# Kernel tuning notes

Measured on AMD Instinct MI355X. Metric: run time of the kernel, lower is better.

Reference implementation:

```python
import jax, jax.numpy as jnp
import numpy as np
from jax.scipy.special import gammaln

INTERVAL_STEPS = (1, -1, -3, 3, 4, -4)
MARGIN = 0.5


def _build_transition(S):
    # T[f, t, i] = 1 if t == f + interval_steps[i], else 0 (within support)
    T = np.zeros((S, S, len(INTERVAL_STEPS)), dtype=np.float32)
    for i, s in enumerate(INTERVAL_STEPS):
        if s > 0:
            f = np.arange(0, S - s)
        else:
            f = np.arange(-s, S)
        T[f, f + s, i] = 1.0
    return jnp.asarray(T)


def _forward(data, log_weights):
    n_data, C = data.shape
    S = int(np.ceil((2 * MARGIN + 1) * C))              # n_dist_support = 256
    center = int(np.round((MARGIN + 0.5) * C))           # reference_center = 128
    down = -min(min(INTERVAL_STEPS), 0)
    up = max(max(INTERVAL_STEPS), 0)
    n_iters = int(np.ceil(max(center / down, (S - center) / up))) + 1  # 33
    T = _build_transition(S)

    # Poisson-weighted Markov diffusion
    w = jnp.exp(log_weights)
    rate = w.sum(axis=1)                                 # [d]
    p = w / rate[:, None]                                # [d, i] interval step probs
    log_rate = jnp.log(rate)
    run0 = jnp.zeros((n_data, S), data.dtype).at[:, center].set(1.0)
    acc0 = jnp.zeros((n_data, S), data.dtype)

    def diff_step(carry, n):
        acc, run = carry
        step_prob = jnp.exp(n * log_rate - rate - gammaln(n + 1.0))  # Poisson pmf(n)
        acc = acc + step_prob[:, None] * run
        # einsum('fti,di,df->dt') done as two controlled contractions
        tmp = jnp.einsum('fti,df->dti', T, run)          # [d, t, i]
        run = jnp.einsum('dti,di->dt', tmp, p)           # [d, t]
        return (acc, run), None

    (acc, _), _ = jax.lax.scan(diff_step, (acc0, run0),
                               jnp.arange(n_iters, dtype=data.dtype))
    icd = acc / acc.sum(axis=1, keepdims=True)           # [d, S]

    # match distributions: min over shifts of DKL(data || normalized slice)
    n_shifts = S - C + 1
    pz = jnp.isclose(data, 0.0)
    safe_p = jnp.where(pz, 1.0, data)
    plogp = jnp.where(pz, 0.0, data * jnp.log(safe_p))   # [d, C]

    def match_step(carry, shift):
        best_loss, best_dist = carry
        d = jax.lax.dynamic_slice_in_dim(icd, shift, C, axis=1)
        d = d / d.sum(axis=1, keepdims=True)
        logq = jnp.log(jnp.maximum(d, 1e-38))            # guard fp32 underflow at edges
        loss = (plogp - jnp.where(pz, 0.0, data * logq)).sum(axis=1)
        cond = loss < best_loss
        return (jnp.where(cond, loss, best_loss),
                jnp.where(cond[:, None], d, best_dist)), None

    init = (jnp.full((n_data,), jnp.inf, data.dtype), jnp.zeros_like(data))
    (matched_loss, matched_dist), _ = jax.lax.scan(match_step, init, jnp.arange(n_shifts))
    return matched_loss


def setup_inputs() -> dict:
    key = jax.random.key(0)
    k1, k2 = jax.random.split(key)
    u = jax.random.uniform(k1, (4096, 128), jnp.float32)
    data = u / u.sum(axis=1, keepdims=True)              # rows are distributions
    # small weights -> Poisson rates ~6, so cum prob is allclose(1) before iter 33,
    # matching the original module's break-at-effective_min_iterations behavior
    log_weights = 0.1 * jax.random.normal(k2, (4096, 6), jnp.float32)
    return {"data": data, "log_weights": log_weights}


def reference(data, log_weights):
    return _forward(data, log_weights)
```

## Files before the change

kernel.cpp:

```cpp
#include <hip/hip_runtime.h>
#include <math.h>

#define NC      128
#define NSTATE  256
#define NITERS  33
#define NSTEPS  6
#define RPB     4
#define CL2     (-126.22347f)
#define LN2     (0.6931471805599453f)

#define DPP_WAVE_SHL1 0x130
#define DPP_WAVE_SHR1 0x138

__device__ __forceinline__ float dpp_shr1(float x) {
    return __int_as_float(__builtin_amdgcn_update_dpp(
        0, __float_as_int(x), DPP_WAVE_SHR1, 0xf, 0xf, true));
}
__device__ __forceinline__ float dpp_shl1(float x) {
    return __int_as_float(__builtin_amdgcn_update_dpp(
        0, __float_as_int(x), DPP_WAVE_SHL1, 0xf, 0xf, true));
}

__global__ __launch_bounds__(256)
void tonal_diffusion_kernel(const float* __restrict__ data,
                            const float* __restrict__ logw,
                            float* __restrict__ out, int n_rows)
{
    const int wid  = threadIdx.x >> 6;
    const int lane = threadIdx.x & 63;
    const int row  = blockIdx.x * RPB + wid;
    if (row >= n_rows) return;
    const int urow = __builtin_amdgcn_readfirstlane(row);

    __shared__ __align__(16) float licdR_s[RPB][4][NSTATE];
    __shared__ __align__(16) float P_s    [RPB][NSTATE];
    float (* __restrict__ licdR)[NSTATE] = licdR_s[wid];
    float * __restrict__ P               = P_s[wid];

    const float* __restrict__ drow = data + (size_t)urow * NC;

    float rate, p0, p1, p2, p3, p4, p5;
    {
        const float* lw = logw + urow * NSTEPS;
        p0 = expf(lw[0]); p1 = expf(lw[1]); p2 = expf(lw[2]);
        p3 = expf(lw[3]); p4 = expf(lw[4]); p5 = expf(lw[5]);
        rate = ((p0 + p1) + (p2 + p3)) + (p4 + p5);
        const float inv = 1.0f / rate;
        p0 *= inv; p1 *= inv; p2 *= inv; p3 *= inv; p4 *= inv; p5 *= inv;
    }

    const float2 dl = *(const float2*)(drow + 2 * lane);
    float plogp;
    {
        float pl = 0.f;
        if (dl.x > 1e-8f) pl += dl.x * logf(dl.x);
        if (dl.y > 1e-8f) pl += dl.y * logf(dl.y);
        #pragma unroll
        for (int off = 1; off < 64; off <<= 1) pl += __shfl_xor(pl, off, 64);
        plogp = pl;
    }

    float r0 = 0.f, r1 = 0.f, r2 = 0.f, r3 = 0.f;
    if (lane == 32) r0 = 1.0f;
    float a0 = 0.f, a1 = 0.f, a2 = 0.f, a3 = 0.f;
    float sp = expf(-rate);
    #pragma unroll
    for (int n = 0; n < NITERS; ++n) {
        a0 += sp * r0; a1 += sp * r1; a2 += sp * r2; a3 += sp * r3;
        const float L0 = dpp_shr1(r0), L1 = dpp_shr1(r1),
                    L2 = dpp_shr1(r2), L3 = dpp_shr1(r3);
        const float R0 = dpp_shl1(r0), R1 = dpp_shl1(r1),
                    R2 = dpp_shl1(r2), R3 = dpp_shl1(r3);
        const float n0 = p0*L3 + p1*r1 + p2*r3 + p3*L1 + p4*L0 + p5*R0;
        const float n1 = p0*r0 + p1*r2 + p2*R0 + p3*L2 + p4*L1 + p5*R1;
        const float n2 = p0*r1 + p1*r3 + p2*R1 + p3*L3 + p4*L2 + p5*R2;
        const float n3 = p0*r2 + p1*R0 + p2*R2 + p3*r0 + p4*L3 + p5*R3;
        r0 = n0; r1 = n1; r2 = n2; r3 = n3;
        sp = sp * rate * (1.0f / (float)(n + 1));
    }

    {
        const float l0 = log2f(a0), l1 = log2f(a1), l2 = log2f(a2), l3 = log2f(a3);
        const float nl0 = dpp_shl1(l0), nl1 = dpp_shl1(l1), nl2 = dpp_shl1(l2);
        *(float4*)&licdR[0][4 * lane] = make_float4(l0, l1, l2, l3);
        *(float4*)&licdR[1][4 * lane] = make_float4(l1, l2, l3, nl0);
        *(float4*)&licdR[2][4 * lane] = make_float4(l2, l3, nl0, nl1);
        *(float4*)&licdR[3][4 * lane] = make_float4(l3, nl0, nl1, nl2);
    }

    {
        const float s0 = a0, s1 = s0 + a1, s2 = s1 + a2, s3 = s2 + a3;
        float t = s3;
        #pragma unroll
        for (int off = 1; off < 64; off <<= 1) {
            const float u = __shfl_up(t, off, 64);
            if (lane >= off) t += u;
        }
        const float base = t - s3;
        *(float4*)&P[4 * lane] = make_float4(base + s0, base + s1, base + s2, base + s3);
    }

    const int phi = lane & 3;
    const float* __restrict__ lcp = &licdR[phi][lane - phi];
    const float zA = log2f(P[lane + 127] - (lane ? P[lane - 1] : 0.f));
    const float zB = log2f(P[lane + 191] - P[lane + 63]);
    float accA = 0.f, accB = 0.f;
    #pragma unroll 8
    for (int m = 0; m < 16; ++m) {
        const float4 v = *(const float4*)(lcp + 4 * m);
        const int c = 4 * m;
        accA += drow[c + 0] * fmaxf(v.x - zA, CL2);
        accA += drow[c + 1] * fmaxf(v.y - zA, CL2);
        accA += drow[c + 2] * fmaxf(v.z - zA, CL2);
        accA += drow[c + 3] * fmaxf(v.w - zA, CL2);
    }
    #pragma unroll 8
    for (int m = 16; m < 32; ++m) {
        const float4 v = *(const float4*)(lcp + 4 * m);
        const int c = 4 * m;
        accA += drow[c + 0] * fmaxf(v.x - zA, CL2);
        accA += drow[c + 1] * fmaxf(v.y - zA, CL2);
        accA += drow[c + 2] * fmaxf(v.z - zA, CL2);
        accA += drow[c + 3] * fmaxf(v.w - zA, CL2);
        accB += drow[c - 64 + 0] * fmaxf(v.x - zB, CL2);
        accB += drow[c - 64 + 1] * fmaxf(v.y - zB, CL2);
        accB += drow[c - 64 + 2] * fmaxf(v.z - zB, CL2);
        accB += drow[c - 64 + 3] * fmaxf(v.w - zB, CL2);
    }
    #pragma unroll 8
    for (int m = 32; m < 48; ++m) {
        const float4 v = *(const float4*)(lcp + 4 * m);
        const int c = 4 * m - 64;
        accB += drow[c + 0] * fmaxf(v.x - zB, CL2);
        accB += drow[c + 1] * fmaxf(v.y - zB, CL2);
        accB += drow[c + 2] * fmaxf(v.z - zB, CL2);
        accB += drow[c + 3] * fmaxf(v.w - zB, CL2);
    }
    float best = fminf(plogp - LN2 * accA, plogp - LN2 * accB);

    {
        const float z = log2f(P[255] - P[127]);
        const float2 lv = *(const float2*)(&licdR[0][128 + 2 * lane]);
        float part = dl.x * fmaxf(lv.x - z, CL2) + dl.y * fmaxf(lv.y - z, CL2);
        #pragma unroll
        for (int off = 1; off < 64; off <<= 1) part += __shfl_xor(part, off, 64);
        best = fminf(best, plogp - LN2 * part);
    }

    #pragma unroll
    for (int off = 1; off < 64; off <<= 1) best = fminf(best, __shfl_xor(best, off, 64));
    if (lane == 0) out[row] = best;
}

extern "C" void kernel_launch(void* const* d_in, const int* in_sizes, int n_in,
                              void* d_out, int out_size, void* d_ws, size_t ws_size,
                              hipStream_t stream)
{
    const float* data = (const float*)d_in[0];
    const float* logw = (const float*)d_in[1];
    float* out = (float*)d_out;
    const int n_rows = in_sizes[0] / NC;
    const int blocks = (n_rows + RPB - 1) / RPB;
    tonal_diffusion_kernel<<<blocks, 256, 0, stream>>>(data, logw, out, n_rows);
}
```

Measured before the change: 75.27 us.

## Use fast intrinsics, vectorized data loads, occupancy hint and smaller unroll

Replaces expf/logf/log2f with the fast __expf/__logf/__log2f intrinsics. The matching loops now load the data row as float4 (uniform scalar loads) instead of individual floats. The unroll factor drops from 8 to 4, and launch_bounds gains a minimum-blocks hint of 4 to steer register allocation. The fast intrinsics lose accuracy on denormal and near-zero inputs, which matters for the log of tiny diffusion probabilities.

```diff
diff --git a/kernel.cpp b/kernel.cpp
--- a/kernel.cpp
+++ b/kernel.cpp
@@ -21,7 +21,7 @@
         0, __float_as_int(x), DPP_WAVE_SHL1, 0xf, 0xf, true));
 }
 
-__global__ __launch_bounds__(256)
+__global__ __launch_bounds__(256, 4)
 void tonal_diffusion_kernel(const float* __restrict__ data,
                             const float* __restrict__ logw,
                             float* __restrict__ out, int n_rows)
@@ -42,8 +42,8 @@
     float rate, p0, p1, p2, p3, p4, p5;
     {
         const float* lw = logw + urow * NSTEPS;
-        p0 = expf(lw[0]); p1 = expf(lw[1]); p2 = expf(lw[2]);
-        p3 = expf(lw[3]); p4 = expf(lw[4]); p5 = expf(lw[5]);
+        p0 = __expf(lw[0]); p1 = __expf(lw[1]); p2 = __expf(lw[2]);
+        p3 = __expf(lw[3]); p4 = __expf(lw[4]); p5 = __expf(lw[5]);
         rate = ((p0 + p1) + (p2 + p3)) + (p4 + p5);
         const float inv = 1.0f / rate;
         p0 *= inv; p1 *= inv; p2 *= inv; p3 *= inv; p4 *= inv; p5 *= inv;
@@ -53,8 +53,8 @@
     float plogp;
     {
         float pl = 0.f;
-        if (dl.x > 1e-8f) pl += dl.x * logf(dl.x);
-        if (dl.y > 1e-8f) pl += dl.y * logf(dl.y);
+        if (dl.x > 1e-8f) pl += dl.x * __logf(dl.x);
+        if (dl.y > 1e-8f) pl += dl.y * __logf(dl.y);
         #pragma unroll
         for (int off = 1; off < 64; off <<= 1) pl += __shfl_xor(pl, off, 64);
         plogp = pl;
@@ -63,7 +63,7 @@
     float r0 = 0.f, r1 = 0.f, r2 = 0.f, r3 = 0.f;
     if (lane == 32) r0 = 1.0f;
     float a0 = 0.f, a1 = 0.f, a2 = 0.f, a3 = 0.f;
-    float sp = expf(-rate);
+    float sp = __expf(-rate);
     #pragma unroll
     for (int n = 0; n < NITERS; ++n) {
         a0 += sp * r0; a1 += sp * r1; a2 += sp * r2; a3 += sp * r3;
@@ -80,7 +80,8 @@
     }
 
     {
-        const float l0 = log2f(a0), l1 = log2f(a1), l2 = log2f(a2), l3 = log2f(a3);
+        const float l0 = __log2f(a0), l1 = __log2f(a1),
+                    l2 = __log2f(a2), l3 = __log2f(a3);
         const float nl0 = dpp_shl1(l0), nl1 = dpp_shl1(l1), nl2 = dpp_shl1(l2);
         *(float4*)&licdR[0][4 * lane] = make_float4(l0, l1, l2, l3);
         *(float4*)&licdR[1][4 * lane] = make_float4(l1, l2, l3, nl0);
@@ -102,44 +103,45 @@
 
     const int phi = lane & 3;
     const float* __restrict__ lcp = &licdR[phi][lane - phi];
-    const float zA = log2f(P[lane + 127] - (lane ? P[lane - 1] : 0.f));
-    const float zB = log2f(P[lane + 191] - P[lane + 63]);
+    const float zA = __log2f(P[lane + 127] - (lane ? P[lane - 1] : 0.f));
+    const float zB = __log2f(P[lane + 191] - P[lane + 63]);
     float accA = 0.f, accB = 0.f;
-    #pragma unroll 8
+    #pragma unroll 4
     for (int m = 0; m < 16; ++m) {
         const float4 v = *(const float4*)(lcp + 4 * m);
-        const int c = 4 * m;
-        accA += drow[c + 0] * fmaxf(v.x - zA, CL2);
-        accA += drow[c + 1] * fmaxf(v.y - zA, CL2);
-        accA += drow[c + 2] * fmaxf(v.z - zA, CL2);
-        accA += drow[c + 3] * fmaxf(v.w - zA, CL2);
+        const float4 d = *(const float4*)(drow + 4 * m);
+        accA += d.x * fmaxf(v.x - zA, CL2);
+        accA += d.y * fmaxf(v.y - zA, CL2);
+        accA += d.z * fmaxf(v.z - zA, CL2);
+        accA += d.w * fmaxf(v.w - zA, CL2);
     }
-    #pragma unroll 8
+    #pragma unroll 4
     for (int m = 16; m < 32; ++m) {
-        const float4 v = *(const float4*)(lcp + 4 * m);
-        const int c = 4 * m;
-        accA += drow[c + 0] * fmaxf(v.x - zA, CL2);
-        accA += drow[c + 1] * fmaxf(v.y - zA, CL2);
-        accA += drow[c + 2] * fmaxf(v.z - zA, CL2);
-        accA += drow[c + 3] * fmaxf(v.w - zA, CL2);
-        accB += drow[c - 64 + 0] * fmaxf(v.x - zB, CL2);
-        accB += drow[c - 64 + 1] * fmaxf(v.y - zB, CL2);
-        accB += drow[c - 64 + 2] * fmaxf(v.z - zB, CL2);
-        accB += drow[c - 64 + 3] * fmaxf(v.w - zB, CL2);
+        const float4 v  = *(const float4*)(lcp + 4 * m);
+        const float4 dA = *(const float4*)(drow + 4 * m);
+        const float4 dB = *(const float4*)(drow + 4 * m - 64);
+        accA += dA.x * fmaxf(v.x - zA, CL2);
+        accA += dA.y * fmaxf(v.y - zA, CL2);
+        accA += dA.z * fmaxf(v.z - zA, CL2);
+        accA += dA.w * fmaxf(v.w - zA, CL2);
+        accB += dB.x * fmaxf(v.x - zB, CL2);
+        accB += dB.y * fmaxf(v.y - zB, CL2);
+        accB += dB.z * fmaxf(v.z - zB, CL2);
+        accB += dB.w * fmaxf(v.w - zB, CL2);
     }
-    #pragma unroll 8
+    #pragma unroll 4
     for (int m = 32; m < 48; ++m) {
-        const float4 v = *(const float4*)(lcp + 4 * m);
-        const int c = 4 * m - 64;
-        accB += drow[c + 0] * fmaxf(v.x - zB, CL2);
-        accB += drow[c + 1] * fmaxf(v.y - zB, CL2);
-        accB += drow[c + 2] * fmaxf(v.z - zB, CL2);
-        accB += drow[c + 3] * fmaxf(v.w - zB, CL2);
+        const float4 v  = *(const float4*)(lcp + 4 * m);
+        const float4 dB = *(const float4*)(drow + 4 * m - 64);
+        accB += dB.x * fmaxf(v.x - zB, CL2);
+        accB += dB.y * fmaxf(v.y - zB, CL2);
+        accB += dB.z * fmaxf(v.z - zB, CL2);
+        accB += dB.w * fmaxf(v.w - zB, CL2);
     }
     float best = fminf(plogp - LN2 * accA, plogp - LN2 * accB);
 
     {
-        const float z = log2f(P[255] - P[127]);
+        const float z = __log2f(P[255] - P[127]);
         const float2 lv = *(const float2*)(&licdR[0][128 + 2 * lane]);
         float part = dl.x * fmaxf(lv.x - z, CL2) + dl.y * fmaxf(lv.y - z, CL2);
         #pragma unroll
```

Measured after the change: 75.58 us. No clear change (+0.4%).
